# Performance work log

Measured on AMD Instinct MI355X. Metric: run time of the kernel, lower is better.

Reference implementation:

```python
import jax, jax.numpy as jnp
import numpy as np

B, OBS, ACT = 16384, 39, 4
D = 400            # backbone_hidden[-1] == expert_hidden[-1] == task_queries_dim
NE, NT = 8, 10     # num_experts, num_tasks


def setup_inputs() -> dict:
    key = jax.random.key(0)
    ks = jax.random.split(key, 20)
    g = lambda k, shp, fan: jax.random.normal(k, shp, dtype=jnp.float32) / np.sqrt(fan)
    return {
        "obs": jax.random.normal(ks[0], (B, OBS), dtype=jnp.float32),
        "act": jax.random.normal(ks[1], (B, ACT), dtype=jnp.float32),
        "task": jax.random.randint(ks[2], (B,), 0, NT),
        # backbone mlp: [obs+act, 400, 400], relu after each layer
        "bb_w1": g(ks[3], (OBS + ACT, D), OBS + ACT), "bb_b1": jnp.zeros((D,), jnp.float32),
        "bb_w2": g(ks[4], (D, D), D), "bb_b2": jnp.zeros((D,), jnp.float32),
        # 8 expert mlps, stacked: [400 -> 400 -> 400], relu after each layer
        "ex_w1": g(ks[5], (NE, D, D), D), "ex_b1": jnp.zeros((NE, D), jnp.float32),
        "ex_w2": g(ks[6], (NE, D, D), D), "ex_b2": jnp.zeros((NE, D), jnp.float32),
        # attention params
        "key_mat": g(ks[7], (NE, D, D), D),
        "value_mat": g(ks[8], (NE, D, D), D),
        "task_queries": jax.random.normal(ks[9], (NT, D), dtype=jnp.float32),
        # tower mlp: [400, 400, 400, 1], relu on hidden layers, identity output
        "tw_w1": g(ks[10], (D, D), D), "tw_b1": jnp.zeros((D,), jnp.float32),
        "tw_w2": g(ks[11], (D, D), D), "tw_b2": jnp.zeros((D,), jnp.float32),
        "tw_w3": g(ks[12], (D, 1), D), "tw_b3": jnp.zeros((1,), jnp.float32),
    }


def reference(obs, act, task, bb_w1, bb_b1, bb_w2, bb_b2,
              ex_w1, ex_b1, ex_w2, ex_b2,
              key_mat, value_mat, task_queries,
              tw_w1, tw_b1, tw_w2, tw_b2, tw_w3, tw_b3):
    x = jnp.concatenate([obs, act], axis=-1)                       # [B, obs+act]
    h = jax.nn.relu(x @ bb_w1 + bb_b1)
    h = jax.nn.relu(h @ bb_w2 + bb_b2)                             # [B, D]
    # all experts as one batched GEMM: e[n, b, :] = expert_n(h[b])
    e = jax.nn.relu(jnp.einsum('bi,nij->nbj', h, ex_w1) + ex_b1[:, None, :])
    e = jax.nn.relu(jnp.einsum('nbi,nij->nbj', e, ex_w2) + ex_b2[:, None, :])  # [NE, B, D]
    # per-expert key/value projections (einsum 'nij,nj->ni' batched over b)
    vals = jnp.einsum('nij,nbj->bni', value_mat, e)                # [B, NE, D]
    keys = jnp.einsum('nij,nbj->bni', key_mat, e)                  # [B, NE, D]
    q = task_queries[task]                                         # [B, D]
    scores = jnp.einsum('bni,bi->bn', keys, q)                     # [B, NE]
    w = jax.nn.softmax(scores, axis=-1)                            # softmax over experts
    tower_in = jnp.einsum('bn,bni->bi', w, vals)                   # [B, D]
    t = jax.nn.relu(tower_in @ tw_w1 + tw_b1)
    t = jax.nn.relu(t @ tw_w2 + tw_b2)
    qval = t @ tw_w3 + tw_b3                                       # [B, 1]
    return jnp.squeeze(qval, -1)                                   # [B]
```

## Files before the change

### kernel.cpp

```cpp
#include <hip/hip_runtime.h>

typedef _Float16 f16;
typedef f16 f16x8 __attribute__((ext_vector_type(8)));
typedef float f32x4 __attribute__((ext_vector_type(4)));

#define NB 16384
#define D 400
#define DP 416
#define NEXP 8
#define NTASK 10
#define NKT 13

#define MEMFENCE asm volatile("" ::: "memory")
#define BAR() do{ MEMFENCE; __builtin_amdgcn_s_barrier(); MEMFENCE; }while(0)
#define VM(N) asm volatile("s_waitcnt vmcnt(" #N ")" ::: "memory")
#define LGKM0 asm volatile("s_waitcnt lgkmcnt(0)" ::: "memory")

static __device__ __forceinline__ f32x4 mfma16x32(f16x8 a, f16x8 b, f32x4 c){
  return __builtin_amdgcn_mfma_f32_16x16x32_f16(a, b, c, 0, 0, 0);
}
static __device__ __forceinline__ void g2l(const void* g, void* l){
  __builtin_amdgcn_global_load_lds((const __attribute__((address_space(1))) void*)g,
      (__attribute__((address_space(3))) void*)l, 16, 0, 0);
}
static __device__ __forceinline__ f16x8 scale8(f16x8 a, f16 s){
  f16x8 r;
  #pragma unroll
  for (int e=0;e<8;e++) r[e] = a[e]*s;
  return r;
}

static __device__ __forceinline__ void stage_duo(const char* wbase, char* lds, int kt,
                                                 int t0, int dd, int h, int lane){
  const int r = lane >> 3, c = lane & 7, cg = c ^ r;
  g2l(wbase + (size_t)((t0 + dd*2 + (cg>>2))*16 + h*8 + r)*832 + (size_t)kt*64 + (cg&3)*16,
      lds + dd*2048 + h*1024);
}
static __device__ __forceinline__ f16x8 rdB(const f16* buf, int dloc, int t, int lhi, int l15){
  return *(const f16x8*)(buf + dloc*1024 + l15*64 + ((((t*4+lhi) ^ (l15&7)))<<3));
}
static __device__ __forceinline__ f16x8 rdL(const f16* lact, int r, int kt, int lhi){
  int q = kt*4 + lhi;
  int c = (q < 48) ? (q ^ (r&7)) : q;
  return *(const f16x8*)(lact + r*416 + (c<<3));
}
static __device__ __forceinline__ int lact_idx(int r, int col){
  int q = col >> 3;
  int c = (q < 48) ? (q ^ (r&7)) : q;
  return r*416 + (c<<3) + (col&7);
}
static __device__ __forceinline__ void stageB4(const char* wb, char* buf, int kt,
                                               int wv, int lane){
  for (int u = wv; u < 26; u += 4) stage_duo(wb, buf, kt, 0, u>>1, u&1, lane);
}


__global__ void k_build_x(const float* __restrict__ obs, const float* __restrict__ act,
                          f16* __restrict__ x)
{
  int idx = blockIdx.x*256 + threadIdx.x;
  int b = idx >> 6, c = idx & 63;
  float v = 0.f;
  if (c < 39) v = obs[b*39 + c];
  else if (c < 43) v = act[b*4 + (c - 39)];
  x[idx] = (f16)v;
}

__global__ void k_transpose(const float* __restrict__ in, f16* __restrict__ out,
                            int K, int N, int Kpad, int Npad)
{
  __shared__ float t[32][33];
  int tx = threadIdx.x & 31, ty = threadIdx.x >> 5;
  int n0 = blockIdx.x*32, k0 = blockIdx.y*32;
  in  += (size_t)blockIdx.z * K * N;
  out += (size_t)blockIdx.z * Npad * Kpad;
  #pragma unroll
  for (int r=0;r<4;r++){
    int k = k0 + ty + r*8, nn = n0 + tx;
    t[ty + r*8][tx] = (k < K && nn < N) ? in[(size_t)k*N + nn] : 0.f;
  }
  __syncthreads();
  #pragma unroll
  for (int r=0;r<4;r++){
    int nn = n0 + ty + r*8, kp = k0 + tx;
    if (nn < Npad && kp < Kpad) out[(size_t)nn*Kpad + kp] = (f16)t[tx][ty + r*8];
  }
}

__global__ void k_val_pad(const float* __restrict__ in, f16* __restrict__ out)
{
  int idx = blockIdx.x*256 + threadIdx.x;
  if (idx >= NEXP*DP*DP) return;
  int c = idx % DP, r = (idx / DP) % DP, n = idx / (DP*DP);
  float v = (r < D && c < D) ? in[((size_t)n*D + r)*D + c] : 0.f;
  out[idx] = (f16)v;
}

__global__ void k_kq(const float* __restrict__ key_mat, const float* __restrict__ tq,
                     float* __restrict__ kq)
{
  __shared__ float tqs[NTASK*D];
  int n = blockIdx.x, tid = threadIdx.x;
  for (int i=tid;i<NTASK*D;i+=256) tqs[i] = tq[i];
  __syncthreads();
  float a0[NTASK], a1[NTASK];
  #pragma unroll
  for (int t=0;t<NTASK;t++){ a0[t]=0.f; a1[t]=0.f; }
  const float* km = key_mat + (size_t)n*D*D;
  for (int i=0;i<D;i++){
    float v0 = km[(size_t)i*D + tid];
    float v1 = (tid+256 < D) ? km[(size_t)i*D + tid + 256] : 0.f;
    #pragma unroll
    for (int t=0;t<NTASK;t++){
      float q = tqs[t*D + i];
      a0[t] += v0*q; a1[t] += v1*q;
    }
  }
  #pragma unroll
  for (int t=0;t<NTASK;t++){
    kq[(size_t)n*NTASK*DP + t*DP + tid] = a0[t];
    if (tid+256 < DP) kq[(size_t)n*NTASK*DP + t*DP + tid+256] = (tid+256 < D) ? a1[t] : 0.f;
  }
}


#define MFMA26(a0_, a1_, BUF) do {                                              \
    __builtin_amdgcn_s_setprio(1);                                              \
    _Pragma("unroll")                                                           \
    for (int j=0;j<13;j++){                                                     \
      int tj = ch*13 + j;                                                       \
      f16x8 b = rdB((BUF), tj>>1, tj&1, lhi, l15);                              \
      acc[0][j] = mfma16x32((a0_), b, acc[0][j]);                               \
      acc[1][j] = mfma16x32((a1_), b, acc[1][j]);                               \
    }                                                                           \
    __builtin_amdgcn_s_setprio(0);                                              \
  } while(0)

#define MFMA13(a0_, BUF) do {                                                   \
    __builtin_amdgcn_s_setprio(1);                                              \
    _Pragma("unroll")                                                           \
    for (int j=0;j<13;j++){                                                     \
      int tj = ch*13 + j;                                                       \
      f16x8 b = rdB((BUF), tj>>1, tj&1, lhi, l15);                              \
      acc[j] = mfma16x32((a0_), b, acc[j]);                                     \
    }                                                                           \
    __builtin_amdgcn_s_setprio(0);                                              \
  } while(0)

__global__ __launch_bounds__(256,2) void k_experts(
    const f16* __restrict__ h16, const f16* __restrict__ w1T, const float* __restrict__ b1s,
    const f16* __restrict__ w2T, const float* __restrict__ b2s,
    f16* __restrict__ e16, const float* __restrict__ kqg, const int* __restrict__ task,
    float* __restrict__ scores)
{
  __shared__ f16 bufB[13*1024];
  __shared__ f16 lact[64*416];
  float (*psum)[2] = (float(*)[2])lact;
  const int tid = threadIdx.x, lane = tid & 63, wv = tid >> 6;
  const int l15 = lane & 15, lhi = lane >> 4;
  const int rh = wv >> 1, ch = wv & 1;
  const int n = blockIdx.x;
  const int rowbase = blockIdx.y * 64;
  const f32x4 Z4 = {0,0,0,0};
  f32x4 acc[2][13];

  const char* wb1 = (const char*)(w1T + (size_t)n*DP*DP);
  const char* wb2 = (const char*)(w2T + (size_t)n*DP*DP);
  const f16* Ab = h16 + (size_t)(rowbase + rh*32 + l15)*DP;

  #pragma unroll
  for (int j=0;j<13;j++){ acc[0][j]=Z4; acc[1][j]=Z4; }
  f16x8 a0 = *(const f16x8*)(Ab + lhi*8);
  f16x8 a1 = *(const f16x8*)(Ab + 16*DP + lhi*8);
  stageB4(wb1, (char*)bufB, 0, wv, lane);
  for (int kt=0; kt<NKT; kt++){
    VM(0); BAR();
    MFMA26(a0, a1, bufB);
    BAR();
    if (kt < NKT-1){
      a0 = *(const f16x8*)(Ab + (kt+1)*32 + lhi*8);
      a1 = *(const f16x8*)(Ab + 16*DP + (kt+1)*32 + lhi*8);
      stageB4(wb1, (char*)bufB, kt+1, wv, lane);
    }
  }
  stageB4(wb2, (char*)bufB, 0, wv, lane);
  #pragma unroll
  for (int j=0;j<13;j++){
    int col = (ch*13+j)*16 + l15;
    float bv = (col<D)? b1s[n*D+col] : 0.f;
    #pragma unroll
    for (int ar=0;ar<2;ar++)
      #pragma unroll
      for (int rr=0;rr<4;rr++){
        float v = acc[ar][j][rr] + bv; v = v>0.f?v:0.f;
        lact[lact_idx(rh*32+ar*16+lhi*4+rr, col)] = (f16)v;
      }
  }
  LGKM0;

  #pragma unroll
  for (int j=0;j<13;j++){ acc[0][j]=Z4; acc[1][j]=Z4; }
  for (int kt=0; kt<NKT; kt++){
    VM(0); BAR();
    f16x8 x0 = rdL(lact, rh*32 + l15, kt, lhi);
    f16x8 x1 = rdL(lact, rh*32 + 16 + l15, kt, lhi);
    MFMA26(x0, x1, bufB);
    BAR();
    if (kt < NKT-1) stageB4(wb2, (char*)bufB, kt+1, wv, lane);
  }
  const float* kqp[2][4];
  const float* kqb = kqg + (size_t)n*NTASK*DP;
  #pragma unroll
  for (int ar=0;ar<2;ar++)
    #pragma unroll
    for (int rr=0;rr<4;rr++){
      int grow = rowbase + rh*32 + ar*16 + lhi*4 + rr;
      kqp[ar][rr] = kqb + (size_t)task[grow]*DP;
    }
  float p_[2][4] = {{0,0,0,0},{0,0,0,0}};
  #pragma unroll
  for (int j=0;j<13;j++){
    int col = (ch*13+j)*16 + l15;
    float bv = (col<D)? b2s[n*D+col] : 0.f;
    #pragma unroll
    for (int ar=0;ar<2;ar++)
      #pragma unroll
      for (int rr=0;rr<4;rr++){
        float v = acc[ar][j][rr] + bv; v = v>0.f?v:0.f;
        e16[((size_t)n*NB + rowbase + rh*32+ar*16+lhi*4+rr)*DP + col] = (f16)v;
        p_[ar][rr] += v * kqp[ar][rr][col];
      }
  }
  #pragma unroll
  for (int ar=0;ar<2;ar++)
    #pragma unroll
    for (int rr=0;rr<4;rr++){
      float p = p_[ar][rr];
      p += __shfl_xor(p, 1, 64);
      p += __shfl_xor(p, 2, 64);
      p += __shfl_xor(p, 4, 64);
      p += __shfl_xor(p, 8, 64);
      if (l15 == 0) psum[rh*32+ar*16+lhi*4+rr][ch] = p;
    }
  LGKM0; BAR();
  if (tid < 64) scores[(size_t)(rowbase + tid)*NEXP + n] = psum[tid][0] + psum[tid][1];
}

__global__ __launch_bounds__(256,2) void k_backbone(
    const f16* __restrict__ x, const f16* __restrict__ w1T, const float* __restrict__ b1,
    const f16* __restrict__ w2T, const float* __restrict__ b2, f16* __restrict__ h16)
{
  __shared__ f16 bufB[13*1024];
  __shared__ f16 lact[32*416];
  const int tid = threadIdx.x, lane = tid & 63, wv = tid >> 6;
  const int l15 = lane & 15, lhi = lane >> 4;
  const int rh = wv >> 1, ch = wv & 1;
  const int rowbase = blockIdx.x * 32;
  const f32x4 Z4 = {0,0,0,0};
  f32x4 acc[13];

  const f16* Ab = x + (size_t)(rowbase + rh*16 + l15)*64;

  #pragma unroll
  for (int j=0;j<13;j++) acc[j]=Z4;
  f16x8 a0 = *(const f16x8*)(Ab + lhi*8);
  stageB4((const char*)w1T, (char*)bufB, 0, wv, lane);
  #pragma unroll
  for (int kt=0; kt<2; kt++){
    VM(0); BAR();
    MFMA13(a0, bufB);
    BAR();
    if (kt == 0){
      a0 = *(const f16x8*)(Ab + 32 + lhi*8);
      stageB4((const char*)w1T, (char*)bufB, 1, wv, lane);
    }
  }
  stageB4((const char*)w2T, (char*)bufB, 0, wv, lane);
  #pragma unroll
  for (int j=0;j<13;j++){
    int col = (ch*13+j)*16 + l15;
    float bv = (col<D)? b1[col] : 0.f;
    #pragma unroll
    for (int rr=0;rr<4;rr++){
      float v = acc[j][rr] + bv; v = v>0.f?v:0.f;
      lact[lact_idx(rh*16+lhi*4+rr, col)] = (f16)v;
    }
  }
  LGKM0;

  #pragma unroll
  for (int j=0;j<13;j++) acc[j]=Z4;
  for (int kt=0; kt<NKT; kt++){
    VM(0); BAR();
    f16x8 x0 = rdL(lact, rh*16 + l15, kt, lhi);
    MFMA13(x0, bufB);
    BAR();
    if (kt < NKT-1) stageB4((const char*)w2T, (char*)bufB, kt+1, wv, lane);
  }
  #pragma unroll
  for (int j=0;j<13;j++){
    int col = (ch*13+j)*16 + l15;
    float bv = (col<D)? b2[col] : 0.f;
    #pragma unroll
    for (int rr=0;rr<4;rr++){
      float v = acc[j][rr] + bv; v = v>0.f?v:0.f;
      h16[(size_t)(rowbase + rh*16+lhi*4+rr)*DP + col] = (f16)v;
    }
  }
}

__global__ __launch_bounds__(256,2) void k_attn(
    const f16* __restrict__ e16, const f16* __restrict__ valT,
    const float* __restrict__ scores, f16* __restrict__ ti16)
{
  __shared__ f16 bufB[2][7*1024];
  __shared__ float wsm[64*NEXP];
  const int tid = threadIdx.x, lane = tid & 63, wv = tid >> 6;
  const int l15 = lane & 15, lhi = lane >> 4;
  const int cb = blockIdx.x;
  const int rowbase = blockIdx.y * 64;
  const int nd = cb ? 6 : 7;
  const int t0 = cb * 14;
  const f32x4 Z4 = {0,0,0,0};
  f32x4 acc[14];
  #pragma unroll
  for (int j=0;j<14;j++) acc[j]=Z4;

  if (tid < 64){
    const float* sr = scores + (size_t)(rowbase + tid)*NEXP;
    float s[8]; float m = -1e30f;
    #pragma unroll
    for (int k=0;k<8;k++){ s[k]=sr[k]; m = fmaxf(m, s[k]); }
    float sum = 0.f;
    #pragma unroll
    for (int k=0;k<8;k++){ s[k] = expf(s[k]-m); sum += s[k]; }
    float inv = 1.f/sum;
    #pragma unroll
    for (int k=0;k<8;k++) wsm[tid*NEXP + k] = s[k]*inv;
  }

  const f16* Arow = e16 + (size_t)(rowbase + wv*16 + l15)*DP;

  #define STAGE_V(n_, k_, BUFC) do {                                            \
    const char* vb_ = (const char*)(valT + (size_t)(n_)*DP*DP);                 \
    for (int u = wv; u < nd*2; u += 4)                                          \
      stage_duo(vb_, (BUFC), (k_), t0, u>>1, u&1, lane);                        \
  } while(0)

  STAGE_V(0, 0, (char*)bufB[0]);
  f16x8 a = *(const f16x8*)(Arow + lhi*8);
  LGKM0; BAR();

  for (int n=0;n<NEXP;n++){
    for (int kt=0;kt<NKT;kt++){
      int s = n*NKT + kt;
      f16x8 an = a;
      if (s < NEXP*NKT-1){
        int n2 = (kt==NKT-1)? n+1 : n, k2 = (kt==NKT-1)? 0 : kt+1;
        STAGE_V(n2, k2, (char*)bufB[(s+1)&1]);
        an = *(const f16x8*)(Arow + (size_t)n2*NB*DP + k2*32 + lhi*8);
        if (cb == 0 && wv < 2) { VM(5); } else { VM(4); }
      } else { VM(0); }
      BAR();
      const f16* bb = bufB[s&1];
      f16 wn = (f16)wsm[(wv*16+l15)*NEXP + n];
      f16x8 as = scale8(a, wn);
      __builtin_amdgcn_s_setprio(1);
      #pragma unroll
      for (int dd=0;dd<7;dd++) if (dd<nd){
        f16x8 b0 = rdB(bb, dd, 0, lhi, l15);
        f16x8 b1 = rdB(bb, dd, 1, lhi, l15);
        acc[dd*2]   = mfma16x32(as, b0, acc[dd*2]);
        acc[dd*2+1] = mfma16x32(as, b1, acc[dd*2+1]);
      }
      __builtin_amdgcn_s_setprio(0);
      BAR();
      a = an;
    }
  }
  #pragma unroll
  for (int dd=0;dd<7;dd++) if (dd<nd)
    #pragma unroll
    for (int t2=0;t2<2;t2++){
      int j = dd*2+t2;
      int col = (t0 + j)*16 + l15;
      #pragma unroll
      for (int rr=0;rr<4;rr++)
        ti16[(size_t)(rowbase + wv*16 + lhi*4 + rr)*DP + col] = (f16)acc[j][rr];
    }
}

__global__ __launch_bounds__(256,2) void k_mlp3(
    const f16* __restrict__ ti16,
    const f16* __restrict__ tw1T, const float* __restrict__ tb1,
    const f16* __restrict__ tw2T, const float* __restrict__ tb2,
    const float* __restrict__ tw3, const float* __restrict__ tb3,
    float* __restrict__ out)
{
  __shared__ f16 bufB[13*1024];
  __shared__ f16 lact[32*416];
  float (*psum)[2] = (float(*)[2])lact;
  const int tid = threadIdx.x, lane = tid & 63, wv = tid >> 6;
  const int l15 = lane & 15, lhi = lane >> 4;
  const int rh = wv >> 1, ch = wv & 1;
  const int rowbase = blockIdx.x * 32;
  const f32x4 Z4 = {0,0,0,0};
  f32x4 acc[13];

  const f16* Ab = ti16 + (size_t)(rowbase + rh*16 + l15)*DP;

  #pragma unroll
  for (int j=0;j<13;j++) acc[j]=Z4;
  f16x8 a0 = *(const f16x8*)(Ab + lhi*8);
  stageB4((const char*)tw1T, (char*)bufB, 0, wv, lane);
  for (int kt=0; kt<NKT; kt++){
    VM(0); BAR();
    MFMA13(a0, bufB);
    BAR();
    if (kt < NKT-1){
      a0 = *(const f16x8*)(Ab + (kt+1)*32 + lhi*8);
      stageB4((const char*)tw1T, (char*)bufB, kt+1, wv, lane);
    }
  }
  stageB4((const char*)tw2T, (char*)bufB, 0, wv, lane);
  #pragma unroll
  for (int j=0;j<13;j++){
    int col = (ch*13+j)*16 + l15;
    float bv = (col<D)? tb1[col] : 0.f;
    #pragma unroll
    for (int rr=0;rr<4;rr++){
      float v = acc[j][rr] + bv; v = v>0.f?v:0.f;
      lact[lact_idx(rh*16+lhi*4+rr, col)] = (f16)v;
    }
  }
  LGKM0;

  #pragma unroll
  for (int j=0;j<13;j++) acc[j]=Z4;
  for (int kt=0; kt<NKT; kt++){
    VM(0); BAR();
    f16x8 x0 = rdL(lact, rh*16 + l15, kt, lhi);
    MFMA13(x0, bufB);
    BAR();
    if (kt < NKT-1) stageB4((const char*)tw2T, (char*)bufB, kt+1, wv, lane);
  }
  float p_[4] = {0,0,0,0};
  #pragma unroll
  for (int j=0;j<13;j++){
    int col = (ch*13+j)*16 + l15;
    float bv = (col<D)? tb2[col] : 0.f;
    float w3 = (col<D)? tw3[col] : 0.f;
    #pragma unroll
    for (int rr=0;rr<4;rr++){
      float v = acc[j][rr] + bv; v = v>0.f?v:0.f;
      p_[rr] += v * w3;
    }
  }
  #pragma unroll
  for (int rr=0;rr<4;rr++){
    float p = p_[rr];
    p += __shfl_xor(p, 1, 64);
    p += __shfl_xor(p, 2, 64);
    p += __shfl_xor(p, 4, 64);
    p += __shfl_xor(p, 8, 64);
    if (l15 == 0) psum[rh*16+lhi*4+rr][ch] = p;
  }
  LGKM0; BAR();
  if (tid < 32) out[rowbase + tid] = psum[tid][0] + psum[tid][1] + tb3[0];
}


extern "C" void kernel_launch(void* const* d_in, const int* in_sizes, int n_in,
                              void* d_out, int out_size, void* d_ws, size_t ws_size,
                              hipStream_t stream)
{
  const float* obs     = (const float*)d_in[0];
  const float* act     = (const float*)d_in[1];
  const int*   task    = (const int*)  d_in[2];
  const float* bb_w1   = (const float*)d_in[3];
  const float* bb_b1   = (const float*)d_in[4];
  const float* bb_w2   = (const float*)d_in[5];
  const float* bb_b2   = (const float*)d_in[6];
  const float* ex_w1   = (const float*)d_in[7];
  const float* ex_b1   = (const float*)d_in[8];
  const float* ex_w2   = (const float*)d_in[9];
  const float* ex_b2   = (const float*)d_in[10];
  const float* key_mat = (const float*)d_in[11];
  const float* val_mat = (const float*)d_in[12];
  const float* tq      = (const float*)d_in[13];
  const float* tw_w1   = (const float*)d_in[14];
  const float* tw_b1   = (const float*)d_in[15];
  const float* tw_w2   = (const float*)d_in[16];
  const float* tw_b2   = (const float*)d_in[17];
  const float* tw_w3   = (const float*)d_in[18];
  const float* tw_b3   = (const float*)d_in[19];

  char* ws = (char*)d_ws;
  size_t off = 0;
  auto alloc = [&](size_t bytes){ void* p = ws + off; off += (bytes + 255) & ~(size_t)255; return p; };
  f16*   x16   = (f16*)  alloc((size_t)NB*64*2);
  f16*   h16   = (f16*)  alloc((size_t)NB*DP*2);
  f16*   e16   = (f16*)  alloc((size_t)NEXP*NB*DP*2);
  f16*   ti16  = (f16*)  alloc((size_t)NB*DP*2);
  float* scors = (float*)alloc((size_t)NB*NEXP*4);
  float* kq    = (float*)alloc((size_t)NEXP*NTASK*DP*4);
  f16*   bbw1T = (f16*)  alloc((size_t)DP*DP*2);
  f16*   bbw2T = (f16*)  alloc((size_t)DP*DP*2);
  f16*   exw1T = (f16*)  alloc((size_t)NEXP*DP*DP*2);
  f16*   exw2T = (f16*)  alloc((size_t)NEXP*DP*DP*2);
  f16*   valT  = (f16*)  alloc((size_t)NEXP*DP*DP*2);
  f16*   tw1T  = (f16*)  alloc((size_t)DP*DP*2);
  f16*   tw2T  = (f16*)  alloc((size_t)DP*DP*2);
  (void)ws_size; (void)in_sizes; (void)n_in; (void)out_size;

  k_build_x<<<NB*64/256, 256, 0, stream>>>(obs, act, x16);
  k_transpose<<<dim3(13,13, 1),  256, 0, stream>>>(bb_w1, bbw1T, 43, D, DP, DP);
  k_transpose<<<dim3(13,13, 1),  256, 0, stream>>>(bb_w2, bbw2T, D, D, DP, DP);
  k_transpose<<<dim3(13,13, 8),  256, 0, stream>>>(ex_w1, exw1T, D, D, DP, DP);
  k_transpose<<<dim3(13,13, 8),  256, 0, stream>>>(ex_w2, exw2T, D, D, DP, DP);
  k_transpose<<<dim3(13,13, 1),  256, 0, stream>>>(tw_w1, tw1T,  D, D, DP, DP);
  k_transpose<<<dim3(13,13, 1),  256, 0, stream>>>(tw_w2, tw2T,  D, D, DP, DP);
  k_val_pad<<<(NEXP*DP*DP + 255)/256, 256, 0, stream>>>(val_mat, valT);
  k_kq<<<NEXP, 256, 0, stream>>>(key_mat, tq, kq);

  k_backbone<<<NB/32, 256, 0, stream>>>(x16, bbw1T, bb_b1, bbw2T, bb_b2, h16);
  k_experts<<<dim3(NEXP, NB/64), 256, 0, stream>>>(h16, exw1T, ex_b1, exw2T, ex_b2,
                                                   e16, kq, task, scors);
  k_attn<<<dim3(2, NB/64), 256, 0, stream>>>(e16, valT, scors, ti16);
  k_mlp3<<<NB/32, 256, 0, stream>>>(ti16, tw1T, tw_b1, tw2T, tw_b2, tw_w3, tw_b3,
                                    (float*)d_out);
}
```

Before: 411.8 us.

## Stage two K-tiles per barrier in backbone, attention and tower kernels; merge transposes

The six weight-transpose launches become a single launch whose z index selects the matrix. The backbone and tower GEMM loops now stage two 32-wide K-tiles per step into a doubled LDS buffer, so they run 7 iterations instead of 13 and need half as many barrier pairs. The attention kernel is rebuilt to match: each wave now computes a 32x7-tile output block, reusing each B fragment across two A rows, and consumes two K-tiles per step. In exchange, prefetch overlap is lost (each load now waits on VM(0) before compute) and LDS use roughly doubles in the 13-tile kernels, which may reduce occupancy.

```diff
diff --git a/kernel.cpp b/kernel.cpp
--- a/kernel.cpp
+++ b/kernel.cpp
@@ -66,24 +66,35 @@
   x[idx] = (f16)v;
 }
 
-__global__ void k_transpose(const float* __restrict__ in, f16* __restrict__ out,
-                            int K, int N, int Kpad, int Npad)
+__global__ void k_transpose_all(
+    const float* __restrict__ bb_w1, const float* __restrict__ bb_w2,
+    const float* __restrict__ ex_w1, const float* __restrict__ ex_w2,
+    const float* __restrict__ tw_w1, const float* __restrict__ tw_w2,
+    f16* __restrict__ bbw1T, f16* __restrict__ bbw2T,
+    f16* __restrict__ exw1T, f16* __restrict__ exw2T,
+    f16* __restrict__ tw1T,  f16* __restrict__ tw2T)
 {
   __shared__ float t[32][33];
+  const int z = blockIdx.z;
+  const float* in; f16* out; int K = D;
+  if (z == 0){ in = bb_w1; out = bbw1T; K = 43; }
+  else if (z == 1){ in = bb_w2; out = bbw2T; }
+  else if (z < 10){ in = ex_w1 + (size_t)(z-2)*D*D;  out = exw1T + (size_t)(z-2)*DP*DP; }
+  else if (z < 18){ in = ex_w2 + (size_t)(z-10)*D*D; out = exw2T + (size_t)(z-10)*DP*DP; }
+  else if (z == 18){ in = tw_w1; out = tw1T; }
+  else { in = tw_w2; out = tw2T; }
   int tx = threadIdx.x & 31, ty = threadIdx.x >> 5;
   int n0 = blockIdx.x*32, k0 = blockIdx.y*32;
-  in  += (size_t)blockIdx.z * K * N;
-  out += (size_t)blockIdx.z * Npad * Kpad;
   #pragma unroll
   for (int r=0;r<4;r++){
     int k = k0 + ty + r*8, nn = n0 + tx;
-    t[ty + r*8][tx] = (k < K && nn < N) ? in[(size_t)k*N + nn] : 0.f;
+    t[ty + r*8][tx] = (k < K && nn < D) ? in[(size_t)k*D + nn] : 0.f;
   }
   __syncthreads();
   #pragma unroll
   for (int r=0;r<4;r++){
     int nn = n0 + ty + r*8, kp = k0 + tx;
-    if (nn < Npad && kp < Kpad) out[(size_t)nn*Kpad + kp] = (f16)t[tx][ty + r*8];
+    if (nn < DP && kp < DP) out[(size_t)nn*DP + kp] = (f16)t[tx][ty + r*8];
   }
 }
 
@@ -145,6 +156,14 @@
       acc[j] = mfma16x32((a0_), b, acc[j]);                                     \
     }                                                                           \
     __builtin_amdgcn_s_setprio(0);                                              \
+  } while(0)
+
+#define STAGE_W(wb_, buf_, p_, full_) do{                                       \
+    int tot_ = (full_) ? 52 : 26;                                               \
+    for (int u = wv; u < tot_; u += 4){                                         \
+      int kh_ = (u >= 26) ? 1 : 0, uu_ = u - (kh_ ? 26 : 0);                    \
+      stage_duo((wb_), (char*)(buf_)[kh_], 2*(p_)+kh_, 0, uu_>>1, uu_&1, lane); \
+    }                                                                           \
   } while(0)
 
 __global__ __launch_bounds__(256,2) void k_experts(
@@ -250,7 +269,7 @@
     const f16* __restrict__ x, const f16* __restrict__ w1T, const float* __restrict__ b1,
     const f16* __restrict__ w2T, const float* __restrict__ b2, f16* __restrict__ h16)
 {
-  __shared__ f16 bufB[13*1024];
+  __shared__ f16 bufB[2][13*1024];
   __shared__ f16 lact[32*416];
   const int tid = threadIdx.x, lane = tid & 63, wv = tid >> 6;
   const int l15 = lane & 15, lhi = lane >> 4;
@@ -263,19 +282,14 @@
 
   #pragma unroll
   for (int j=0;j<13;j++) acc[j]=Z4;
+  STAGE_W((const char*)w1T, bufB, 0, 1);
   f16x8 a0 = *(const f16x8*)(Ab + lhi*8);
-  stageB4((const char*)w1T, (char*)bufB, 0, wv, lane);
-  #pragma unroll
-  for (int kt=0; kt<2; kt++){
-    VM(0); BAR();
-    MFMA13(a0, bufB);
-    BAR();
-    if (kt == 0){
-      a0 = *(const f16x8*)(Ab + 32 + lhi*8);
-      stageB4((const char*)w1T, (char*)bufB, 1, wv, lane);
-    }
-  }
-  stageB4((const char*)w2T, (char*)bufB, 0, wv, lane);
+  f16x8 a1 = *(const f16x8*)(Ab + 32 + lhi*8);
+  VM(0); BAR();
+  MFMA13(a0, bufB[0]);
+  MFMA13(a1, bufB[1]);
+  BAR();
+  STAGE_W((const char*)w2T, bufB, 0, 1);
   #pragma unroll
   for (int j=0;j<13;j++){
     int col = (ch*13+j)*16 + l15;
@@ -290,12 +304,16 @@
 
   #pragma unroll
   for (int j=0;j<13;j++) acc[j]=Z4;
-  for (int kt=0; kt<NKT; kt++){
+  for (int p=0; p<7; p++){
     VM(0); BAR();
-    f16x8 x0 = rdL(lact, rh*16 + l15, kt, lhi);
-    MFMA13(x0, bufB);
+    f16x8 x0 = rdL(lact, rh*16 + l15, 2*p, lhi);
+    MFMA13(x0, bufB[0]);
+    if (p < 6){
+      f16x8 x1 = rdL(lact, rh*16 + l15, 2*p+1, lhi);
+      MFMA13(x1, bufB[1]);
+    }
     BAR();
-    if (kt < NKT-1) stageB4((const char*)w2T, (char*)bufB, kt+1, wv, lane);
+    if (p < 6) STAGE_W((const char*)w2T, bufB, p+1, (p+1)<6);
   }
   #pragma unroll
   for (int j=0;j<13;j++){
@@ -313,18 +331,22 @@
     const f16* __restrict__ e16, const f16* __restrict__ valT,
     const float* __restrict__ scores, f16* __restrict__ ti16)
 {
-  __shared__ f16 bufB[2][7*1024];
+  __shared__ f16 buf[2][7*1024];
   __shared__ float wsm[64*NEXP];
   const int tid = threadIdx.x, lane = tid & 63, wv = tid >> 6;
   const int l15 = lane & 15, lhi = lane >> 4;
+  const int rg = wv >> 1, cg = wv & 1;
   const int cb = blockIdx.x;
   const int rowbase = blockIdx.y * 64;
   const int nd = cb ? 6 : 7;
+  const int ntw = cb ? 6 : 7;
   const int t0 = cb * 14;
   const f32x4 Z4 = {0,0,0,0};
-  f32x4 acc[14];
-  #pragma unroll
-  for (int j=0;j<14;j++) acc[j]=Z4;
+  f32x4 acc[2][7];
+  #pragma unroll
+  for (int a=0;a<2;a++)
+    #pragma unroll
+    for (int j=0;j<7;j++) acc[a][j]=Z4;
 
   if (tid < 64){
     const float* sr = scores + (size_t)(rowbase + tid)*NEXP;
@@ -339,54 +361,71 @@
     for (int k=0;k<8;k++) wsm[tid*NEXP + k] = s[k]*inv;
   }
 
-  const f16* Arow = e16 + (size_t)(rowbase + wv*16 + l15)*DP;
-
-  #define STAGE_V(n_, k_, BUFC) do {                                            \
+  #define STAGE_A(n_, p_) do {                                                  \
     const char* vb_ = (const char*)(valT + (size_t)(n_)*DP*DP);                 \
-    for (int u = wv; u < nd*2; u += 4)                                          \
-      stage_duo(vb_, (BUFC), (k_), t0, u>>1, u&1, lane);                        \
+    int nu_ = nd*2, tot_ = ((p_)<6) ? nd*4 : nd*2;                              \
+    for (int u = wv; u < tot_; u += 4){                                         \
+      int kh_ = (u >= nu_) ? 1 : 0, uu_ = u - (kh_ ? nu_ : 0);                  \
+      stage_duo(vb_, (char*)buf[kh_], 2*(p_)+kh_, t0, uu_>>1, uu_&1, lane);     \
+    }                                                                           \
   } while(0)
 
-  STAGE_V(0, 0, (char*)bufB[0]);
-  f16x8 a = *(const f16x8*)(Arow + lhi*8);
-  LGKM0; BAR();
+  #define LDA_A(n_, kt_, ar_) \
+    (*(const f16x8*)(e16 + ((size_t)(n_)*NB + rowbase + rg*32 + (ar_)*16 + l15)*DP + (kt_)*32 + lhi*8))
+
+  STAGE_A(0, 0);
+  f16x8 aC00 = LDA_A(0,0,0), aC01 = LDA_A(0,0,1);
+  f16x8 aC10 = LDA_A(0,1,0), aC11 = LDA_A(0,1,1);
+  LGKM0;
 
   for (int n=0;n<NEXP;n++){
-    for (int kt=0;kt<NKT;kt++){
-      int s = n*NKT + kt;
-      f16x8 an = a;
-      if (s < NEXP*NKT-1){
-        int n2 = (kt==NKT-1)? n+1 : n, k2 = (kt==NKT-1)? 0 : kt+1;
-        STAGE_V(n2, k2, (char*)bufB[(s+1)&1]);
-        an = *(const f16x8*)(Arow + (size_t)n2*NB*DP + k2*32 + lhi*8);
-        if (cb == 0 && wv < 2) { VM(5); } else { VM(4); }
-      } else { VM(0); }
+    for (int p=0;p<7;p++){
+      int s = n*7 + p;
+      VM(0); BAR();
+      f16 w0 = (f16)wsm[(rg*32      + l15)*NEXP + n];
+      f16 w1 = (f16)wsm[(rg*32 + 16 + l15)*NEXP + n];
+      {
+        f16x8 as0 = scale8(aC00, w0), as1 = scale8(aC01, w1);
+        __builtin_amdgcn_s_setprio(1);
+        #pragma unroll
+        for (int j=0;j<7;j++) if (j<ntw){
+          int tl = cg*ntw + j;
+          f16x8 b = rdB(buf[0], tl>>1, tl&1, lhi, l15);
+          acc[0][j] = mfma16x32(as0, b, acc[0][j]);
+          acc[1][j] = mfma16x32(as1, b, acc[1][j]);
+        }
+        __builtin_amdgcn_s_setprio(0);
+      }
+      if (p < 6){
+        f16x8 as0 = scale8(aC10, w0), as1 = scale8(aC11, w1);
+        __builtin_amdgcn_s_setprio(1);
+        #pragma unroll
+        for (int j=0;j<7;j++) if (j<ntw){
+          int tl = cg*ntw + j;
+          f16x8 b = rdB(buf[1], tl>>1, tl&1, lhi, l15);
+          acc[0][j] = mfma16x32(as0, b, acc[0][j]);
+          acc[1][j] = mfma16x32(as1, b, acc[1][j]);
+        }
+        __builtin_amdgcn_s_setprio(0);
+      }
       BAR();
-      const f16* bb = bufB[s&1];
-      f16 wn = (f16)wsm[(wv*16+l15)*NEXP + n];
-      f16x8 as = scale8(a, wn);
-      __builtin_amdgcn_s_setprio(1);
-      #pragma unroll
-      for (int dd=0;dd<7;dd++) if (dd<nd){
-        f16x8 b0 = rdB(bb, dd, 0, lhi, l15);
-        f16x8 b1 = rdB(bb, dd, 1, lhi, l15);
-        acc[dd*2]   = mfma16x32(as, b0, acc[dd*2]);
-        acc[dd*2+1] = mfma16x32(as, b1, acc[dd*2+1]);
+      if (s < NEXP*7 - 1){
+        int p2 = (p==6) ? 0 : p+1;
+        int n2 = (p==6) ? n+1 : n;
+        STAGE_A(n2, p2);
+        aC00 = LDA_A(n2, 2*p2,   0); aC01 = LDA_A(n2, 2*p2,   1);
+        if (p2 < 6){ aC10 = LDA_A(n2, 2*p2+1, 0); aC11 = LDA_A(n2, 2*p2+1, 1); }
       }
-      __builtin_amdgcn_s_setprio(0);
-      BAR();
-      a = an;
-    }
-  }
-  #pragma unroll
-  for (int dd=0;dd<7;dd++) if (dd<nd)
-    #pragma unroll
-    for (int t2=0;t2<2;t2++){
-      int j = dd*2+t2;
-      int col = (t0 + j)*16 + l15;
+    }
+  }
+  #pragma unroll
+  for (int ar=0;ar<2;ar++)
+    #pragma unroll
+    for (int j=0;j<7;j++) if (j<ntw){
+      int col = (t0 + cg*ntw + j)*16 + l15;
       #pragma unroll
       for (int rr=0;rr<4;rr++)
-        ti16[(size_t)(rowbase + wv*16 + lhi*4 + rr)*DP + col] = (f16)acc[j][rr];
+        ti16[(size_t)(rowbase + rg*32 + ar*16 + lhi*4 + rr)*DP + col] = (f16)acc[ar][j][rr];
     }
 }
 
@@ -397,7 +436,7 @@
     const float* __restrict__ tw3, const float* __restrict__ tb3,
     float* __restrict__ out)
 {
-  __shared__ f16 bufB[13*1024];
+  __shared__ f16 bufB[2][13*1024];
   __shared__ f16 lact[32*416];
   float (*psum)[2] = (float(*)[2])lact;
   const int tid = threadIdx.x, lane = tid & 63, wv = tid >> 6;
@@ -411,18 +450,21 @@
 
   #pragma unroll
   for (int j=0;j<13;j++) acc[j]=Z4;
+  STAGE_W((const char*)tw1T, bufB, 0, 1);
   f16x8 a0 = *(const f16x8*)(Ab + lhi*8);
-  stageB4((const char*)tw1T, (char*)bufB, 0, wv, lane);
-  for (int kt=0; kt<NKT; kt++){
+  f16x8 a1 = *(const f16x8*)(Ab + 32 + lhi*8);
+  for (int p=0; p<7; p++){
     VM(0); BAR();
-    MFMA13(a0, bufB);
+    MFMA13(a0, bufB[0]);
+    if (p < 6) MFMA13(a1, bufB[1]);
     BAR();
-    if (kt < NKT-1){
-      a0 = *(const f16x8*)(Ab + (kt+1)*32 + lhi*8);
-      stageB4((const char*)tw1T, (char*)bufB, kt+1, wv, lane);
-    }
-  }
-  stageB4((const char*)tw2T, (char*)bufB, 0, wv, lane);
+    if (p < 6){
+      STAGE_W((const char*)tw1T, bufB, p+1, (p+1)<6);
+      a0 = *(const f16x8*)(Ab + (2*p+2)*32 + lhi*8);
+      if (p+1 < 6) a1 = *(const f16x8*)(Ab + (2*p+3)*32 + lhi*8);
+    }
+  }
+  STAGE_W((const char*)tw2T, bufB, 0, 1);
   #pragma unroll
   for (int j=0;j<13;j++){
     int col = (ch*13+j)*16 + l15;
@@ -437,12 +479,16 @@
 
   #pragma unroll
   for (int j=0;j<13;j++) acc[j]=Z4;
-  for (int kt=0; kt<NKT; kt++){
+  for (int p=0; p<7; p++){
     VM(0); BAR();
-    f16x8 x0 = rdL(lact, rh*16 + l15, kt, lhi);
-    MFMA13(x0, bufB);
+    f16x8 x0 = rdL(lact, rh*16 + l15, 2*p, lhi);
+    MFMA13(x0, bufB[0]);
+    if (p < 6){
+      f16x8 x1 = rdL(lact, rh*16 + l15, 2*p+1, lhi);
+      MFMA13(x1, bufB[1]);
+    }
     BAR();
-    if (kt < NKT-1) stageB4((const char*)tw2T, (char*)bufB, kt+1, wv, lane);
+    if (p < 6) STAGE_W((const char*)tw2T, bufB, p+1, (p+1)<6);
   }
   float p_[4] = {0,0,0,0};
   #pragma unroll
@@ -514,12 +560,9 @@
   (void)ws_size; (void)in_sizes; (void)n_in; (void)out_size;
 
   k_build_x<<<NB*64/256, 256, 0, stream>>>(obs, act, x16);
-  k_transpose<<<dim3(13,13, 1),  256, 0, stream>>>(bb_w1, bbw1T, 43, D, DP, DP);
-  k_transpose<<<dim3(13,13, 1),  256, 0, stream>>>(bb_w2, bbw2T, D, D, DP, DP);
-  k_transpose<<<dim3(13,13, 8),  256, 0, stream>>>(ex_w1, exw1T, D, D, DP, DP);
-  k_transpose<<<dim3(13,13, 8),  256, 0, stream>>>(ex_w2, exw2T, D, D, DP, DP);
-  k_transpose<<<dim3(13,13, 1),  256, 0, stream>>>(tw_w1, tw1T,  D, D, DP, DP);
-  k_transpose<<<dim3(13,13, 1),  256, 0, stream>>>(tw_w2, tw2T,  D, D, DP, DP);
+  k_transpose_all<<<dim3(13,13,20), 256, 0, stream>>>(
+      bb_w1, bb_w2, ex_w1, ex_w2, tw_w1, tw_w2,
+      bbw1T, bbw2T, exw1T, exw2T, tw1T, tw2T);
   k_val_pad<<<(NEXP*DP*DP + 255)/256, 256, 0, stream>>>(val_mat, valT);
   k_kq<<<NEXP, 256, 0, stream>>>(key_mat, tq, kq);
 
```

After: 400.5 us. 1.03x faster.
